# Kernel tuning notes

Hardware: AMD Instinct MI355X
Metric: run time of the kernel (lower is better)

## Reference

```python
import jax, jax.numpy as jnp
import numpy as np

B, N, C, H = 2, 4096, 384, 6
HD = C // H          # 64
HALF = C // 2        # 192 = 3 pose heads * HD
MLP_H = 4 * C        # 1536
EPS = 1e-5


def _ln(x, g, b):
    m = jnp.mean(x, axis=-1, keepdims=True)
    v = jnp.mean((x - m) ** 2, axis=-1, keepdims=True)
    return (x - m) * jax.lax.rsqrt(v + EPS) * g + b


def setup_inputs() -> dict:
    key = jax.random.key(0)
    ks = jax.random.split(key, 6)
    s = 0.02
    return {
        "x": jax.random.normal(ks[0], (B, N, C), dtype=jnp.float32),
        "qkv_w": jax.random.normal(ks[1], (3 * C, C), dtype=jnp.float32) * s,
        "proj_w": jax.random.normal(ks[2], (C, HALF), dtype=jnp.float32) * s,
        "proj_b": jnp.zeros((C,), jnp.float32),
        "gamma1": jnp.ones((C,), jnp.float32),
        "beta1": jnp.zeros((C,), jnp.float32),
        "gamma2": jnp.ones((C,), jnp.float32),
        "beta2": jnp.zeros((C,), jnp.float32),
        "fc1_w": jax.random.normal(ks[3], (MLP_H, C), dtype=jnp.float32) * s,
        "fc1_b": jnp.zeros((MLP_H,), jnp.float32),
        "fc2_w": jax.random.normal(ks[4], (C, MLP_H), dtype=jnp.float32) * s,
        "fc2_b": jnp.zeros((C,), jnp.float32),
    }


def reference(x, qkv_w, proj_w, proj_b, gamma1, beta1, gamma2, beta2,
              fc1_w, fc1_b, fc2_w, fc2_b):
    b, n, c = x.shape
    scale = HD ** -0.5
    # --- attention on pre-norm input ---
    h = _ln(x, gamma1, beta1)
    qkv = (h @ qkv_w.T).reshape(b, n, 3, H, HD).transpose(2, 0, 3, 1, 4)  # [3,B,H,N,HD]
    q, k, v = qkv[0], qkv[1], qkv[2]
    # obj heads 0:3 -> sigmoid attention; pose heads 3:6 -> softmax attention
    attn_obj = jax.nn.sigmoid(jnp.einsum('bhnd,bhmd->bhnm', q[:, :3], k[:, :3]) * scale)
    attn_pose = jax.nn.softmax(jnp.einsum('bhnd,bhmd->bhnm', q[:, 3:], k[:, 3:]) * scale, axis=-1)
    # chained combine: pose-attn applied after obj-attn on pose values
    ctx = jnp.einsum('bhnm,bhmd->bhnd', attn_obj, v[:, 3:])      # [B,3,N,HD]
    ctx = jnp.einsum('bhnm,bhmd->bhnd', attn_pose, ctx)          # [B,3,N,HD]
    ctx = ctx.transpose(0, 2, 1, 3).reshape(b, n, HALF)          # [B,N,C/2]
    x = x + (ctx @ proj_w.T + proj_b)
    # --- MLP ---
    h2 = _ln(x, gamma2, beta2)
    mlp = jax.nn.gelu(h2 @ fc1_w.T + fc1_b, approximate=False) @ fc2_w.T + fc2_b
    return (x + mlp, attn_obj)
```

## Files before the change

### kernel.cpp

```cpp
#include <hip/hip_runtime.h>
#include <hip/hip_bf16.h>
#include <cmath>


typedef __hip_bfloat16 bf16;
typedef __attribute__((ext_vector_type(8))) short short8;
typedef __attribute__((ext_vector_type(4))) short s16x4;
typedef __attribute__((ext_vector_type(4))) float f32x4;

#define MFMA16(a, b, c) __builtin_amdgcn_mfma_f32_16x16x32_bf16((a), (b), (c), 0, 0, 0)

__device__ __forceinline__ void async16(const void* g, void* l) {
  __builtin_amdgcn_global_load_lds(
      (const __attribute__((address_space(1))) void*)g,
      (__attribute__((address_space(3))) void*)l, 16, 0, 0);
}

__device__ __forceinline__ short f2bs(float v) {
  union { bf16 b; short s; } u;
  u.b = __float2bfloat16(v);
  return u.s;
}

template <bool FIRST>
__global__ __launch_bounds__(256) void ln_fwd(const float* __restrict__ x,
                                              const float* __restrict__ gamma,
                                              const float* __restrict__ beta,
                                              bf16* __restrict__ out,
                                              const float* __restrict__ w0,
                                              const float* __restrict__ w1,
                                              const float* __restrict__ w2,
                                              const float* __restrict__ w3,
                                              bf16* __restrict__ o0, bf16* __restrict__ o1,
                                              bf16* __restrict__ o2, bf16* __restrict__ o3) {
  const int bx = blockIdx.x;
  if (FIRST) {
    if (bx >= 2048) {
      int i = (bx - 2048) * 256 + threadIdx.x;
      const int n0 = 442368 / 4, n1 = 73728 / 4, n2 = 589824 / 4, n3 = 589824 / 4;
      const float* src;
      bf16* dst;
      if (i < n0) { src = w0; dst = o0; }
      else if ((i -= n0) < n1) { src = w1; dst = o1; }
      else if ((i -= n1) < n2) { src = w2; dst = o2; }
      else { i -= n2; src = w3; dst = o3; }
      f32x4 v = *(const f32x4*)(src + (size_t)i * 4);
      s16x4 o;
#pragma unroll
      for (int e = 0; e < 4; ++e) o[e] = f2bs(v[e]);
      *(s16x4*)(dst + (size_t)i * 4) = o;
      return;
    }
  }
  const int row = bx * 4 + (threadIdx.x >> 6);
  const int l = threadIdx.x & 63;
  const float* xr = x + (size_t)row * 384;
  float v[6];
  float s = 0.f, q = 0.f;
#pragma unroll
  for (int i = 0; i < 6; ++i) {
    v[i] = xr[l + i * 64];
    s += v[i];
    q += v[i] * v[i];
  }
#pragma unroll
  for (int m = 1; m < 64; m <<= 1) {
    s += __shfl_xor(s, m);
    q += __shfl_xor(q, m);
  }
  float mean = s * (1.0f / 384.0f);
  float var = q * (1.0f / 384.0f) - mean * mean;
  float rstd = rsqrtf(var + 1e-5f);
  bf16* orow = out + (size_t)row * 384;
#pragma unroll
  for (int i = 0; i < 6; ++i)
    orow[l + i * 64] = __float2bfloat16((v[i] - mean) * rstd * gamma[l + i * 64] + beta[l + i * 64]);
}

template <int EPI>
__global__ __launch_bounds__(256) void gemm128(const bf16* __restrict__ A,
                                               const bf16* __restrict__ Bm, int M, int N, int K,
                                               const float* __restrict__ bias,
                                               bf16* __restrict__ outb) {
  __shared__ __attribute__((aligned(16))) short As[128][64];
  __shared__ __attribute__((aligned(16))) short Bs[128][64];
  const int t = threadIdx.x;
  const int l = t & 63;
  const int w = t >> 6;
  const int wm = w >> 1, wn = w & 1;
  const int bm = blockIdx.y * 128, bn = blockIdx.x * 128;

  f32x4 acc[4][4] = {};
  const int r8 = t >> 3;
  const int c8 = (t & 7) * 8;
  const bf16* Ab = A + (size_t)(bm + r8) * K + c8;
  const bf16* Bb = Bm + (size_t)(bn + r8) * K + c8;

  for (int kt = 0; kt < K; kt += 64) {
    __syncthreads();
#pragma unroll
    for (int i = 0; i < 4; ++i)
      async16(Ab + (size_t)(i * 32) * K + kt, &As[i * 32 + r8][c8]);
#pragma unroll
    for (int i = 0; i < 4; ++i)
      async16(Bb + (size_t)(i * 32) * K + kt, &Bs[i * 32 + r8][c8]);
    __syncthreads();
#pragma unroll
    for (int ks = 0; ks < 2; ++ks) {
      short8 a[4], b[4];
#pragma unroll
      for (int i = 0; i < 4; ++i)
        a[i] = *(const short8*)&As[wm * 64 + i * 16 + (l & 15)][ks * 32 + (l >> 4) * 8];
#pragma unroll
      for (int i = 0; i < 4; ++i)
        b[i] = *(const short8*)&Bs[wn * 64 + i * 16 + (l & 15)][ks * 32 + (l >> 4) * 8];
#pragma unroll
      for (int i = 0; i < 4; ++i)
#pragma unroll
        for (int j = 0; j < 4; ++j) acc[i][j] = MFMA16(a[i], b[j], acc[i][j]);
    }
  }

#pragma unroll
  for (int i = 0; i < 4; ++i) {
#pragma unroll
    for (int j = 0; j < 4; ++j) {
#pragma unroll
      for (int r = 0; r < 4; ++r) {
        int row = bm + wm * 64 + i * 16 + (l >> 4) * 4 + r;
        int col = bn + wn * 64 + j * 16 + (l & 15);
        float v = acc[i][j][r];
        if (EPI == 0) {
          int three = col / 384;
          int rem = col - three * 384;
          int head = rem >> 6;
          int hd = rem & 63;
          int bb = row >> 12;
          int n = row & 4095;
          const size_t QSZ = (size_t)2 * 6 * 4096 * 64;
          if (three < 2) {
            size_t di = ((((size_t)three * 2 + bb) * 6 + head) * 4096 + n) * 64 + hd;
            outb[di] = __float2bfloat16(v);
          } else {
            size_t di = 2 * QSZ + (((size_t)bb * 6 + head) * 64 + hd) * 4096 + n;
            outb[di] = __float2bfloat16(v);
          }
        } else {
          float u = v + bias[col];
          float z = 0.7978845608f * (u + 0.044715f * u * u * u);
          float e = __builtin_amdgcn_exp2f(z * 2.885390082f);
          float th = 1.0f - 2.0f * __builtin_amdgcn_rcpf(e + 1.0f);
          outb[(size_t)row * N + col] = __float2bfloat16(0.5f * u * (1.0f + th));
        }
      }
    }
  }
}

__global__ __launch_bounds__(256) void gemm64sq(const bf16* __restrict__ A,
                                                const bf16* __restrict__ Bm, int M, int N, int K,
                                                const float* __restrict__ bias,
                                                const float* __restrict__ resid,
                                                float* __restrict__ outf) {
  __shared__ __attribute__((aligned(16))) short As[2][64][64];
  __shared__ __attribute__((aligned(16))) short Bs[2][64][64];
  const int t = threadIdx.x;
  const int l = t & 63;
  const int w = t >> 6;
  const int wm = w >> 1, wn = w & 1;
  const int bm = blockIdx.y * 64, bn = blockIdx.x * 64;
  const int r8 = t >> 3, c8 = (t & 7) * 8;

  const bf16* Ab = A + (size_t)(bm + r8) * K + c8;
  const bf16* Bb = Bm + (size_t)(bn + r8) * K + c8;

  f32x4 acc[2][2] = {};

  auto stage = [&](int kt, int bf) {
    async16(Ab + kt, &As[bf][r8][c8]);
    async16(Ab + (size_t)32 * K + kt, &As[bf][32 + r8][c8]);
    async16(Bb + kt, &Bs[bf][r8][c8]);
    async16(Bb + (size_t)32 * K + kt, &Bs[bf][32 + r8][c8]);
  };

  stage(0, 0);
  int bf = 0;
  for (int kt = 0; kt < K; kt += 64) {
    __syncthreads();
    if (kt + 64 < K) stage(kt + 64, bf ^ 1);
#pragma unroll
    for (int ks = 0; ks < 2; ++ks) {
      short8 a[2], b[2];
#pragma unroll
      for (int i = 0; i < 2; ++i)
        a[i] = *(const short8*)&As[bf][wm * 32 + i * 16 + (l & 15)][ks * 32 + (l >> 4) * 8];
#pragma unroll
      for (int j = 0; j < 2; ++j)
        b[j] = *(const short8*)&Bs[bf][wn * 32 + j * 16 + (l & 15)][ks * 32 + (l >> 4) * 8];
#pragma unroll
      for (int i = 0; i < 2; ++i)
#pragma unroll
        for (int j = 0; j < 2; ++j) acc[i][j] = MFMA16(a[i], b[j], acc[i][j]);
    }
    bf ^= 1;
  }

#pragma unroll
  for (int i = 0; i < 2; ++i) {
#pragma unroll
    for (int j = 0; j < 2; ++j) {
#pragma unroll
      for (int r = 0; r < 4; ++r) {
        int row = bm + wm * 32 + i * 16 + (l >> 4) * 4 + r;
        int col = bn + wn * 32 + j * 16 + (l & 15);
        size_t di = (size_t)row * N + col;
        outf[di] = acc[i][j][r] + bias[col] + resid[di];
      }
    }
  }
}

template <int MODE>
__global__ __launch_bounds__(256) void attn_fused(const bf16* __restrict__ qkvb,
                                                  const bf16* __restrict__ vsrc_base,
                                                  float* __restrict__ aout,
                                                  float* __restrict__ part,
                                                  float* __restrict__ lpart) {
  const int bh = blockIdx.z, b = bh / 3, h = bh - b * 3;
  const int row0 = blockIdx.x * 128;
  const int cbase = blockIdx.y * 1024;
  const int t = threadIdx.x, l = t & 63, w = t >> 6;

  const size_t HSZ = (size_t)4096 * 64;
  const size_t QSZ = (size_t)2 * 6 * 4096 * 64;
  const int head = (MODE == 0) ? h : h + 3;
  const bf16* qp = qkvb + (size_t)(b * 6 + head) * HSZ;
  const bf16* kp = qkvb + QSZ + (size_t)(b * 6 + head) * HSZ;
  const bf16* vbase = (MODE == 0)
      ? qkvb + 2 * QSZ + (size_t)((b * 6 + h + 3) * 64) * 4096
      : vsrc_base + (size_t)(bh * 64) * 4096;

  __shared__ __attribute__((aligned(16))) short Ks[2][64][64];
  __shared__ __attribute__((aligned(16))) short Vs[2][64][64];
  __shared__ __attribute__((aligned(16))) float Sf[4][16][68];

  short8 aq[2][2];
#pragma unroll
  for (int rf = 0; rf < 2; ++rf) {
    int qrow = row0 + rf * 64 + w * 16 + (l & 15);
    const bf16* qq = qp + (size_t)qrow * 64 + (l >> 4) * 8;
    aq[rf][0] = *(const short8*)(qq);
    aq[rf][1] = *(const short8*)(qq + 32);
  }

  const int r8 = t >> 3, c8 = (t & 7) * 8;
  const int sc = c8 ^ ((r8 & 7) * 8);

  auto stage = [&](int ct, int bf) {
    const bf16* kb = kp + (size_t)(cbase + ct * 64) * 64;
    async16(kb + (size_t)r8 * 64 + sc, &Ks[bf][r8][c8]);
    async16(kb + (size_t)(32 + r8) * 64 + sc, &Ks[bf][32 + r8][c8]);
    const bf16* vb = vbase + cbase + ct * 64;
    async16(vb + (size_t)r8 * 4096 + sc, &Vs[bf][r8][c8]);
    async16(vb + (size_t)(32 + r8) * 4096 + sc, &Vs[bf][32 + r8][c8]);
  };

  f32x4 cacc[2][4] = {};
  float lp[2][4] = {};
  const float K1 = -0.18033688f;
  const float K2 = 0.18033688f;

  float* sfw = &Sf[w][0][0];
  stage(0, 0);
  int bf = 0;
  for (int ct = 0; ct < 16; ++ct) {
    __syncthreads();
    if (ct < 15) stage(ct + 1, bf ^ 1);

    f32x4 sacc[2][4] = {};
#pragma unroll
    for (int ks = 0; ks < 2; ++ks) {
      short8 bk[4];
#pragma unroll
      for (int j = 0; j < 4; ++j) {
        int rr = j * 16 + (l & 15);
        int ec = (ks * 32 + (l >> 4) * 8) ^ ((rr & 7) * 8);
        bk[j] = *(const short8*)&Ks[bf][rr][ec];
      }
      __builtin_amdgcn_s_setprio(1);
#pragma unroll
      for (int rf = 0; rf < 2; ++rf)
#pragma unroll
        for (int j = 0; j < 4; ++j)
          sacc[rf][j] = MFMA16(aq[rf][ks], bk[j], sacc[rf][j]);
      __builtin_amdgcn_s_setprio(0);
    }

    short8 pa[2][2];
#pragma unroll
    for (int rf = 0; rf < 2; ++rf) {
#pragma unroll
      for (int j = 0; j < 4; ++j) {
#pragma unroll
        for (int r = 0; r < 4; ++r) {
          float s = sacc[rf][j][r];
          float v;
          if (MODE == 0) {
            v = __builtin_amdgcn_rcpf(1.0f + __builtin_amdgcn_exp2f(s * K1));
          } else {
            v = __builtin_amdgcn_exp2f(s * K2);
            lp[rf][r] += v;
          }
          sfw[((l >> 4) * 4 + r) * 68 + j * 16 + (l & 15)] = v;
        }
      }
#pragma unroll
      for (int ks = 0; ks < 2; ++ks) {
        const float* sp = &sfw[(l & 15) * 68 + ks * 32 + (l >> 4) * 8];
        f32x4 f0 = *(const f32x4*)sp;
        f32x4 f1 = *(const f32x4*)(sp + 4);
        short8 a;
#pragma unroll
        for (int e = 0; e < 4; ++e) a[e] = f2bs(f0[e]);
#pragma unroll
        for (int e = 0; e < 4; ++e) a[4 + e] = f2bs(f1[e]);
        pa[rf][ks] = a;
      }
      if (MODE == 0) {
        float* ab = aout + (size_t)bh * 4096 * 4096 +
                    (size_t)(row0 + rf * 64 + w * 16) * 4096 + cbase + ct * 64;
#pragma unroll
        for (int i = 0; i < 4; ++i) {
          f32x4 vv = *(const f32x4*)&sfw[(4 * i + (l >> 4)) * 68 + (l & 15) * 4];
          *(f32x4*)(ab + (size_t)(4 * i + (l >> 4)) * 4096 + (l & 15) * 4) = vv;
        }
      }
    }

#pragma unroll
    for (int ks = 0; ks < 2; ++ks) {
      short8 bv[4];
#pragma unroll
      for (int j = 0; j < 4; ++j) {
        int rr = j * 16 + (l & 15);
        int ec = (ks * 32 + (l >> 4) * 8) ^ ((rr & 7) * 8);
        bv[j] = *(const short8*)&Vs[bf][rr][ec];
      }
      __builtin_amdgcn_s_setprio(1);
#pragma unroll
      for (int rf = 0; rf < 2; ++rf)
#pragma unroll
        for (int j = 0; j < 4; ++j)
          cacc[rf][j] = MFMA16(pa[rf][ks], bv[j], cacc[rf][j]);
      __builtin_amdgcn_s_setprio(0);
    }
    bf ^= 1;
  }

#pragma unroll
  for (int rf = 0; rf < 2; ++rf) {
    float* pb = part + ((size_t)(blockIdx.y * 6 + bh) * 4096 + row0 + rf * 64 + w * 16) * 64;
#pragma unroll
    for (int j = 0; j < 4; ++j)
#pragma unroll
      for (int r = 0; r < 4; ++r)
        pb[(size_t)((l >> 4) * 4 + r) * 64 + j * 16 + (l & 15)] = cacc[rf][j][r];
  }

  if (MODE == 1) {
#pragma unroll
    for (int rf = 0; rf < 2; ++rf) {
#pragma unroll
      for (int r = 0; r < 4; ++r) {
#pragma unroll
        for (int m = 1; m < 16; m <<= 1) lp[rf][r] += __shfl_xor(lp[rf][r], m);
      }
      if ((l & 15) == 0) {
        float* lb = lpart + (size_t)(blockIdx.y * 6 + bh) * 4096 + row0 + rf * 64 + w * 16 + (l >> 4) * 4;
#pragma unroll
        for (int r = 0; r < 4; ++r) lb[r] = lp[rf][r];
      }
    }
  }
}

__global__ __launch_bounds__(256) void reduce_obj(const float* __restrict__ part,
                                                  bf16* __restrict__ ctx1T) {
  const int bh = blockIdx.y, n0 = blockIdx.x * 64, t = threadIdx.x;
  __shared__ short S[64][66];
  const int nr = t >> 2, h0 = (t & 3) * 16;
  const size_t CS = (size_t)6 * 4096 * 64;
  const float* p0 = part + ((size_t)bh * 4096 + n0 + nr) * 64 + h0;
#pragma unroll
  for (int q = 0; q < 4; ++q) {
    f32x4 s = {};
#pragma unroll
    for (int c = 0; c < 4; ++c) s += *(const f32x4*)(p0 + c * CS + q * 4);
#pragma unroll
    for (int e = 0; e < 4; ++e) S[nr][h0 + q * 4 + e] = f2bs(s[e]);
  }
  __syncthreads();
  const int hd = t >> 2, nb = (t & 3) * 16;
  short8 o0, o1;
#pragma unroll
  for (int k = 0; k < 8; ++k) o0[k] = S[nb + k][hd];
#pragma unroll
  for (int k = 0; k < 8; ++k) o1[k] = S[nb + 8 + k][hd];
  short* dst = (short*)(ctx1T + ((size_t)bh * 64 + hd) * 4096 + n0 + nb);
  *(short8*)dst = o0;
  *(short8*)(dst + 8) = o1;
}

__global__ __launch_bounds__(256) void reduce_pose(const float* __restrict__ part,
                                                   const float* __restrict__ lpart,
                                                   bf16* __restrict__ ctxf) {
  const int idx = blockIdx.x * 256 + threadIdx.x;
  const int hd4 = idx & 15;
  const int n = (idx >> 4) & 4095;
  const int bh = idx >> 16;
  const size_t CS = (size_t)6 * 4096 * 64, CL = (size_t)6 * 4096;
  f32x4 s = {};
  float lt = 0.f;
#pragma unroll
  for (int c = 0; c < 4; ++c) {
    s += *(const f32x4*)(part + c * CS + ((size_t)bh * 4096 + n) * 64 + hd4 * 4);
    lt += lpart[c * CL + (size_t)bh * 4096 + n];
  }
  float inv = 1.0f / lt;
  int b = bh / 3, h = bh - b * 3;
  s16x4 o;
#pragma unroll
  for (int e = 0; e < 4; ++e) o[e] = f2bs(s[e] * inv);
  *(s16x4*)(ctxf + ((size_t)b * 4096 + n) * 192 + h * 64 + hd4 * 4) = o;
}

extern "C" void kernel_launch(void* const* d_in, const int* in_sizes, int n_in,
                              void* d_out, int out_size, void* d_ws, size_t ws_size,
                              hipStream_t stream) {
  const float* x      = (const float*)d_in[0];
  const float* qkv_w  = (const float*)d_in[1];
  const float* proj_w = (const float*)d_in[2];
  const float* proj_b = (const float*)d_in[3];
  const float* gamma1 = (const float*)d_in[4];
  const float* beta1  = (const float*)d_in[5];
  const float* gamma2 = (const float*)d_in[6];
  const float* beta2  = (const float*)d_in[7];
  const float* fc1_w  = (const float*)d_in[8];
  const float* fc1_b  = (const float*)d_in[9];
  const float* fc2_w  = (const float*)d_in[10];
  const float* fc2_b  = (const float*)d_in[11];

  float* out_x = (float*)d_out;
  float* out_attn = out_x + (size_t)2 * 4096 * 384;

  char* ws = (char*)d_ws;
  size_t off = 0;
  auto alloc = [&](size_t bytes) -> void* {
    void* p = ws + off;
    off += (bytes + 255) & ~(size_t)255;
    return p;
  };
  bf16* qkv_w_b  = (bf16*)alloc((size_t)1152 * 384 * 2);
  bf16* proj_w_b = (bf16*)alloc((size_t)384 * 192 * 2);
  bf16* fc1_w_b  = (bf16*)alloc((size_t)1536 * 384 * 2);
  bf16* fc2_w_b  = (bf16*)alloc((size_t)384 * 1536 * 2);
  bf16* h1    = (bf16*)alloc((size_t)8192 * 384 * 2);
  bf16* qkvb  = (bf16*)alloc((size_t)3 * 2 * 6 * 4096 * 64 * 2);
  float* c1p  = (float*)alloc((size_t)4 * 6 * 4096 * 64 * 4);
  float* cpp  = (float*)alloc((size_t)4 * 6 * 4096 * 64 * 4);
  float* lpp  = (float*)alloc((size_t)4 * 6 * 4096 * 4);
  bf16* ctx1T = (bf16*)alloc((size_t)6 * 64 * 4096 * 2);
  bf16* ctxf  = (bf16*)alloc((size_t)2 * 4096 * 192 * 2);
  float* x2   = (float*)alloc((size_t)8192 * 384 * 4);
  bf16* h2    = (bf16*)alloc((size_t)8192 * 384 * 2);
  bf16* h3    = (bf16*)alloc((size_t)8192 * 1536 * 2);

  ln_fwd<true><<<3704, 256, 0, stream>>>(x, gamma1, beta1, h1,
                                         qkv_w, proj_w, fc1_w, fc2_w,
                                         qkv_w_b, proj_w_b, fc1_w_b, fc2_w_b);

  gemm128<0><<<dim3(9, 64), 256, 0, stream>>>(h1, qkv_w_b, 8192, 1152, 384,
                                              nullptr, qkvb);

  attn_fused<0><<<dim3(32, 4, 6), 256, 0, stream>>>(qkvb, nullptr, out_attn, c1p, nullptr);
  reduce_obj<<<dim3(64, 6), 256, 0, stream>>>(c1p, ctx1T);
  attn_fused<1><<<dim3(32, 4, 6), 256, 0, stream>>>(qkvb, ctx1T, nullptr, cpp, lpp);
  reduce_pose<<<1536, 256, 0, stream>>>(cpp, lpp, ctxf);

  gemm64sq<<<dim3(6, 128), 256, 0, stream>>>(ctxf, proj_w_b, 8192, 384, 192,
                                             proj_b, x, x2);
  ln_fwd<false><<<2048, 256, 0, stream>>>(x2, gamma2, beta2, h2,
                                          nullptr, nullptr, nullptr, nullptr,
                                          nullptr, nullptr, nullptr, nullptr);
  gemm128<2><<<dim3(12, 64), 256, 0, stream>>>(h2, fc1_w_b, 8192, 1536, 384,
                                               fc1_b, h3);
  gemm64sq<<<dim3(6, 128), 256, 0, stream>>>(h3, fc2_w_b, 8192, 384, 1536,
                                             fc2_b, x2, out_x);
}
```

Measured before the change: 295.7 us.

## Drop key-split in attention and fuse partial reductions into attention epilogue

Each attention block now covers 64 query rows over all keys instead of 128 rows over a quarter of the keys. The output is normalised and written as bf16 directly from the epilogue, and the separate reduce kernels and fp32 partial buffers are removed. This removes partial-sum global traffic and two launches. In exchange it halves per-wave MFMA reuse of each staged K/V tile and reduces the grid to fewer blocks, which may hurt occupancy and load balance.

```diff
diff --git a/kernel.cpp b/kernel.cpp
--- a/kernel.cpp
+++ b/kernel.cpp
@@ -224,11 +224,9 @@
 __global__ __launch_bounds__(256) void attn_fused(const bf16* __restrict__ qkvb,
                                                   const bf16* __restrict__ vsrc_base,
                                                   float* __restrict__ aout,
-                                                  float* __restrict__ part,
-                                                  float* __restrict__ lpart) {
-  const int bh = blockIdx.z, b = bh / 3, h = bh - b * 3;
-  const int row0 = blockIdx.x * 128;
-  const int cbase = blockIdx.y * 1024;
+                                                  bf16* __restrict__ outd) {
+  const int bh = blockIdx.y, b = bh / 3, h = bh - b * 3;
+  const int row0 = blockIdx.x * 64;
   const int t = threadIdx.x, l = t & 63, w = t >> 6;
 
   const size_t HSZ = (size_t)4096 * 64;
@@ -243,41 +241,41 @@
   __shared__ __attribute__((aligned(16))) short Ks[2][64][64];
   __shared__ __attribute__((aligned(16))) short Vs[2][64][64];
   __shared__ __attribute__((aligned(16))) float Sf[4][16][68];
-
-  short8 aq[2][2];
-#pragma unroll
-  for (int rf = 0; rf < 2; ++rf) {
-    int qrow = row0 + rf * 64 + w * 16 + (l & 15);
+  __shared__ float Ls[4][16];
+
+  short8 aq[2];
+  {
+    int qrow = row0 + w * 16 + (l & 15);
     const bf16* qq = qp + (size_t)qrow * 64 + (l >> 4) * 8;
-    aq[rf][0] = *(const short8*)(qq);
-    aq[rf][1] = *(const short8*)(qq + 32);
+    aq[0] = *(const short8*)(qq);
+    aq[1] = *(const short8*)(qq + 32);
   }
 
   const int r8 = t >> 3, c8 = (t & 7) * 8;
   const int sc = c8 ^ ((r8 & 7) * 8);
 
   auto stage = [&](int ct, int bf) {
-    const bf16* kb = kp + (size_t)(cbase + ct * 64) * 64;
+    const bf16* kb = kp + (size_t)(ct * 64) * 64;
     async16(kb + (size_t)r8 * 64 + sc, &Ks[bf][r8][c8]);
     async16(kb + (size_t)(32 + r8) * 64 + sc, &Ks[bf][32 + r8][c8]);
-    const bf16* vb = vbase + cbase + ct * 64;
+    const bf16* vb = vbase + ct * 64;
     async16(vb + (size_t)r8 * 4096 + sc, &Vs[bf][r8][c8]);
     async16(vb + (size_t)(32 + r8) * 4096 + sc, &Vs[bf][32 + r8][c8]);
   };
 
-  f32x4 cacc[2][4] = {};
-  float lp[2][4] = {};
+  f32x4 cacc[4] = {};
+  float lp[4] = {0.f, 0.f, 0.f, 0.f};
   const float K1 = -0.18033688f;
   const float K2 = 0.18033688f;
 
   float* sfw = &Sf[w][0][0];
   stage(0, 0);
   int bf = 0;
-  for (int ct = 0; ct < 16; ++ct) {
-    __syncthreads();
-    if (ct < 15) stage(ct + 1, bf ^ 1);
-
-    f32x4 sacc[2][4] = {};
+  for (int ct = 0; ct < 64; ++ct) {
+    __syncthreads();
+    if (ct < 63) stage(ct + 1, bf ^ 1);
+
+    f32x4 sacc[4] = {};
 #pragma unroll
     for (int ks = 0; ks < 2; ++ks) {
       short8 bk[4];
@@ -289,51 +287,47 @@
       }
       __builtin_amdgcn_s_setprio(1);
 #pragma unroll
-      for (int rf = 0; rf < 2; ++rf)
-#pragma unroll
-        for (int j = 0; j < 4; ++j)
-          sacc[rf][j] = MFMA16(aq[rf][ks], bk[j], sacc[rf][j]);
+      for (int j = 0; j < 4; ++j) sacc[j] = MFMA16(aq[ks], bk[j], sacc[j]);
       __builtin_amdgcn_s_setprio(0);
     }
 
-    short8 pa[2][2];
-#pragma unroll
-    for (int rf = 0; rf < 2; ++rf) {
-#pragma unroll
-      for (int j = 0; j < 4; ++j) {
-#pragma unroll
-        for (int r = 0; r < 4; ++r) {
-          float s = sacc[rf][j][r];
-          float v;
-          if (MODE == 0) {
-            v = __builtin_amdgcn_rcpf(1.0f + __builtin_amdgcn_exp2f(s * K1));
-          } else {
-            v = __builtin_amdgcn_exp2f(s * K2);
-            lp[rf][r] += v;
-          }
-          sfw[((l >> 4) * 4 + r) * 68 + j * 16 + (l & 15)] = v;
+#pragma unroll
+    for (int j = 0; j < 4; ++j) {
+#pragma unroll
+      for (int r = 0; r < 4; ++r) {
+        float s = sacc[j][r];
+        float v;
+        if (MODE == 0) {
+          v = __builtin_amdgcn_rcpf(1.0f + __builtin_amdgcn_exp2f(s * K1));
+        } else {
+          v = __builtin_amdgcn_exp2f(s * K2);
+          lp[r] += v;
         }
-      }
-#pragma unroll
-      for (int ks = 0; ks < 2; ++ks) {
-        const float* sp = &sfw[(l & 15) * 68 + ks * 32 + (l >> 4) * 8];
-        f32x4 f0 = *(const f32x4*)sp;
-        f32x4 f1 = *(const f32x4*)(sp + 4);
-        short8 a;
-#pragma unroll
-        for (int e = 0; e < 4; ++e) a[e] = f2bs(f0[e]);
-#pragma unroll
-        for (int e = 0; e < 4; ++e) a[4 + e] = f2bs(f1[e]);
-        pa[rf][ks] = a;
-      }
-      if (MODE == 0) {
-        float* ab = aout + (size_t)bh * 4096 * 4096 +
-                    (size_t)(row0 + rf * 64 + w * 16) * 4096 + cbase + ct * 64;
-#pragma unroll
-        for (int i = 0; i < 4; ++i) {
-          f32x4 vv = *(const f32x4*)&sfw[(4 * i + (l >> 4)) * 68 + (l & 15) * 4];
-          *(f32x4*)(ab + (size_t)(4 * i + (l >> 4)) * 4096 + (l & 15) * 4) = vv;
-        }
+        sfw[((l >> 4) * 4 + r) * 68 + j * 16 + (l & 15)] = v;
+      }
+    }
+
+    short8 pa[2];
+#pragma unroll
+    for (int ks = 0; ks < 2; ++ks) {
+      const float* sp = &sfw[(l & 15) * 68 + ks * 32 + (l >> 4) * 8];
+      f32x4 f0 = *(const f32x4*)sp;
+      f32x4 f1 = *(const f32x4*)(sp + 4);
+      short8 a;
+#pragma unroll
+      for (int e = 0; e < 4; ++e) a[e] = f2bs(f0[e]);
+#pragma unroll
+      for (int e = 0; e < 4; ++e) a[4 + e] = f2bs(f1[e]);
+      pa[ks] = a;
+    }
+
+    if (MODE == 0) {
+      float* ab = aout + (size_t)bh * 4096 * 4096 +
+                  (size_t)(row0 + w * 16) * 4096 + ct * 64;
+#pragma unroll
+      for (int i = 0; i < 4; ++i) {
+        f32x4 vv = *(const f32x4*)&sfw[(4 * i + (l >> 4)) * 68 + (l & 15) * 4];
+        *(f32x4*)(ab + (size_t)(4 * i + (l >> 4)) * 4096 + (l & 15) * 4) = vv;
       }
     }
 
@@ -348,90 +342,58 @@
       }
       __builtin_amdgcn_s_setprio(1);
 #pragma unroll
-      for (int rf = 0; rf < 2; ++rf)
-#pragma unroll
-        for (int j = 0; j < 4; ++j)
-          cacc[rf][j] = MFMA16(pa[rf][ks], bv[j], cacc[rf][j]);
+      for (int j = 0; j < 4; ++j) cacc[j] = MFMA16(pa[ks], bv[j], cacc[j]);
       __builtin_amdgcn_s_setprio(0);
     }
     bf ^= 1;
   }
 
-#pragma unroll
-  for (int rf = 0; rf < 2; ++rf) {
-    float* pb = part + ((size_t)(blockIdx.y * 6 + bh) * 4096 + row0 + rf * 64 + w * 16) * 64;
+  if (MODE == 0) {
+    __syncthreads();
+    short(*S)[66] = (short(*)[66]) & Ks[0][0][0];
 #pragma unroll
     for (int j = 0; j < 4; ++j)
 #pragma unroll
       for (int r = 0; r < 4; ++r)
-        pb[(size_t)((l >> 4) * 4 + r) * 64 + j * 16 + (l & 15)] = cacc[rf][j][r];
-  }
-
-  if (MODE == 1) {
-#pragma unroll
-    for (int rf = 0; rf < 2; ++rf) {
-#pragma unroll
-      for (int r = 0; r < 4; ++r) {
-#pragma unroll
-        for (int m = 1; m < 16; m <<= 1) lp[rf][r] += __shfl_xor(lp[rf][r], m);
-      }
-      if ((l & 15) == 0) {
-        float* lb = lpart + (size_t)(blockIdx.y * 6 + bh) * 4096 + row0 + rf * 64 + w * 16 + (l >> 4) * 4;
-#pragma unroll
-        for (int r = 0; r < 4; ++r) lb[r] = lp[rf][r];
-      }
-    }
-  }
-}
-
-__global__ __launch_bounds__(256) void reduce_obj(const float* __restrict__ part,
-                                                  bf16* __restrict__ ctx1T) {
-  const int bh = blockIdx.y, n0 = blockIdx.x * 64, t = threadIdx.x;
-  __shared__ short S[64][66];
-  const int nr = t >> 2, h0 = (t & 3) * 16;
-  const size_t CS = (size_t)6 * 4096 * 64;
-  const float* p0 = part + ((size_t)bh * 4096 + n0 + nr) * 64 + h0;
-#pragma unroll
-  for (int q = 0; q < 4; ++q) {
-    f32x4 s = {};
-#pragma unroll
-    for (int c = 0; c < 4; ++c) s += *(const f32x4*)(p0 + c * CS + q * 4);
-#pragma unroll
-    for (int e = 0; e < 4; ++e) S[nr][h0 + q * 4 + e] = f2bs(s[e]);
-  }
-  __syncthreads();
-  const int hd = t >> 2, nb = (t & 3) * 16;
-  short8 o0, o1;
-#pragma unroll
-  for (int k = 0; k < 8; ++k) o0[k] = S[nb + k][hd];
-#pragma unroll
-  for (int k = 0; k < 8; ++k) o1[k] = S[nb + 8 + k][hd];
-  short* dst = (short*)(ctx1T + ((size_t)bh * 64 + hd) * 4096 + n0 + nb);
-  *(short8*)dst = o0;
-  *(short8*)(dst + 8) = o1;
-}
-
-__global__ __launch_bounds__(256) void reduce_pose(const float* __restrict__ part,
-                                                   const float* __restrict__ lpart,
-                                                   bf16* __restrict__ ctxf) {
-  const int idx = blockIdx.x * 256 + threadIdx.x;
-  const int hd4 = idx & 15;
-  const int n = (idx >> 4) & 4095;
-  const int bh = idx >> 16;
-  const size_t CS = (size_t)6 * 4096 * 64, CL = (size_t)6 * 4096;
-  f32x4 s = {};
-  float lt = 0.f;
-#pragma unroll
-  for (int c = 0; c < 4; ++c) {
-    s += *(const f32x4*)(part + c * CS + ((size_t)bh * 4096 + n) * 64 + hd4 * 4);
-    lt += lpart[c * CL + (size_t)bh * 4096 + n];
-  }
-  float inv = 1.0f / lt;
-  int b = bh / 3, h = bh - b * 3;
-  s16x4 o;
-#pragma unroll
-  for (int e = 0; e < 4; ++e) o[e] = f2bs(s[e] * inv);
-  *(s16x4*)(ctxf + ((size_t)b * 4096 + n) * 192 + h * 64 + hd4 * 4) = o;
+        S[w * 16 + (l >> 4) * 4 + r][j * 16 + (l & 15)] = f2bs(cacc[j][r]);
+    __syncthreads();
+    const int hd = t >> 2, nb = (t & 3) * 16;
+    short8 o0, o1;
+#pragma unroll
+    for (int k = 0; k < 8; ++k) o0[k] = S[nb + k][hd];
+#pragma unroll
+    for (int k = 0; k < 8; ++k) o1[k] = S[nb + 8 + k][hd];
+    short* dst = (short*)(outd + ((size_t)bh * 64 + hd) * 4096 + row0 + nb);
+    *(short8*)dst = o0;
+    *(short8*)(dst + 8) = o1;
+  } else {
+#pragma unroll
+    for (int r = 0; r < 4; ++r) {
+#pragma unroll
+      for (int m = 1; m < 16; m <<= 1) lp[r] += __shfl_xor(lp[r], m);
+    }
+    if ((l & 15) == 0) {
+#pragma unroll
+      for (int r = 0; r < 4; ++r) Ls[w][(l >> 4) * 4 + r] = lp[r];
+    }
+#pragma unroll
+    for (int j = 0; j < 4; ++j)
+#pragma unroll
+      for (int r = 0; r < 4; ++r)
+        sfw[((l >> 4) * 4 + r) * 68 + j * 16 + (l & 15)] = cacc[j][r];
+    const int row = l >> 2, hd0 = (l & 3) * 16;
+    float inv = 1.0f / Ls[w][row];
+    short8 o[2];
+#pragma unroll
+    for (int g = 0; g < 4; ++g) {
+      f32x4 v = *(const f32x4*)&sfw[row * 68 + hd0 + g * 4];
+#pragma unroll
+      for (int e = 0; e < 4; ++e) o[g >> 1][(g & 1) * 4 + e] = f2bs(v[e] * inv);
+    }
+    short* dst = (short*)(outd + ((size_t)b * 4096 + row0 + w * 16 + row) * 192 + h * 64 + hd0);
+    *(short8*)dst = o[0];
+    *(short8*)(dst + 8) = o[1];
+  }
 }
 
 extern "C" void kernel_launch(void* const* d_in, const int* in_sizes, int n_in,
@@ -466,9 +428,6 @@
   bf16* fc2_w_b  = (bf16*)alloc((size_t)384 * 1536 * 2);
   bf16* h1    = (bf16*)alloc((size_t)8192 * 384 * 2);
   bf16* qkvb  = (bf16*)alloc((size_t)3 * 2 * 6 * 4096 * 64 * 2);
-  float* c1p  = (float*)alloc((size_t)4 * 6 * 4096 * 64 * 4);
-  float* cpp  = (float*)alloc((size_t)4 * 6 * 4096 * 64 * 4);
-  float* lpp  = (float*)alloc((size_t)4 * 6 * 4096 * 4);
   bf16* ctx1T = (bf16*)alloc((size_t)6 * 64 * 4096 * 2);
   bf16* ctxf  = (bf16*)alloc((size_t)2 * 4096 * 192 * 2);
   float* x2   = (float*)alloc((size_t)8192 * 384 * 4);
@@ -482,10 +441,8 @@
   gemm128<0><<<dim3(9, 64), 256, 0, stream>>>(h1, qkv_w_b, 8192, 1152, 384,
                                               nullptr, qkvb);
 
-  attn_fused<0><<<dim3(32, 4, 6), 256, 0, stream>>>(qkvb, nullptr, out_attn, c1p, nullptr);
-  reduce_obj<<<dim3(64, 6), 256, 0, stream>>>(c1p, ctx1T);
-  attn_fused<1><<<dim3(32, 4, 6), 256, 0, stream>>>(qkvb, ctx1T, nullptr, cpp, lpp);
-  reduce_pose<<<1536, 256, 0, stream>>>(cpp, lpp, ctxf);
+  attn_fused<0><<<dim3(64, 6), 256, 0, stream>>>(qkvb, nullptr, out_attn, ctx1T);
+  attn_fused<1><<<dim3(64, 6), 256, 0, stream>>>(qkvb, ctx1T, nullptr, ctxf);
 
   gemm64sq<<<dim3(6, 128), 256, 0, stream>>>(ctxf, proj_w_b, 8192, 384, 192,
                                              proj_b, x, x2);
```

Measured after the change: 309.0 us. 1.04x slower.
